# Kernel tuning notes

Measured on AMD Instinct MI355X. Metric: run time of the kernel, lower is better.

## Reference

```python
import jax, jax.numpy as jnp
import numpy as np

VOCAB = 50257
D = 1024
L = 2
EPS = 1e-6


def _attn_layer(x, Wq, bq, Wk, bk, Wv, bv, Wo, bo):
    # x: [b, n, d]; W*: [d, d] (torch Linear convention y = x @ W.T + b)
    Q = jax.nn.elu(x @ Wq.T + bq) + 1.0
    K = jax.nn.elu(x @ Wk.T + bk) + 1.0
    V = x @ Wv.T + bv
    KV = jnp.einsum('bnd,bne->bde', K, V)              # [b, d, d]
    Z = jnp.einsum('bnd,bd->bn', Q, K.sum(axis=1) + EPS)  # [b, n]
    context = jnp.einsum('bnd,bde->bne', Q, KV) / Z[..., None]
    return context @ Wo.T + bo


def setup_inputs() -> dict:
    key = jax.random.key(0)
    ks = jax.random.split(key, 12)
    s = 1.0 / np.sqrt(D)
    inp = {
        'input_ids': jax.random.randint(ks[0], (2, 2048), 0, VOCAB),
        'emb': jax.random.normal(ks[1], (VOCAB, D), jnp.float32) * 0.02,
        'Wq': jax.random.normal(ks[2], (L, D, D), jnp.float32) * s,
        'bq': jnp.zeros((L, D), jnp.float32),
        'Wk': jax.random.normal(ks[3], (L, D, D), jnp.float32) * s,
        'bk': jnp.zeros((L, D), jnp.float32),
        'Wv': jax.random.normal(ks[4], (L, D, D), jnp.float32) * s,
        'bv': jnp.zeros((L, D), jnp.float32),
        'Wo': jax.random.normal(ks[5], (L, D, D), jnp.float32) * s,
        'bo': jnp.zeros((L, D), jnp.float32),
        'W_head': jax.random.normal(ks[6], (VOCAB, D), jnp.float32) * s,
        'b_head': jnp.zeros((VOCAB,), jnp.float32),
    }
    return inp


def reference(input_ids, emb, Wq, bq, Wk, bk, Wv, bv, Wo, bo, W_head, b_head):
    x = emb[input_ids]  # [b, n, d]
    for l in range(L):
        x = _attn_layer(x, Wq[l], bq[l], Wk[l], bk[l], Wv[l], bv[l], Wo[l], bo[l])
    logits = x @ W_head.T + b_head  # [b, n, vocab]
    pooled = x[:, -1]               # [b, d]
    return (logits, pooled)
```

## Files before the change

kernel.cpp:

```cpp
#include <hip/hip_runtime.h>
#include <hip/hip_bf16.h>
#include <math.h>

typedef __bf16 bf8_t __attribute__((ext_vector_type(8)));
typedef __bf16 bf4_t __attribute__((ext_vector_type(4)));
typedef float  f4_t  __attribute__((ext_vector_type(4)));

#define AS_G __attribute__((address_space(1)))
#define AS_L __attribute__((address_space(3)))

static __device__ __forceinline__ void gl_lds16(const __bf16* g, __bf16* l) {
    __builtin_amdgcn_global_load_lds((const AS_G void*)g, (AS_L void*)l, 16, 0, 0);
}

static __device__ __forceinline__ void phase_bar() {
    asm volatile("" ::: "memory");
    __builtin_amdgcn_s_barrier();
    asm volatile("" ::: "memory");
}

enum {
    EPI_NONE = 0,
    EPI_BCOL,
    EPI_BCOL_ELU,
    EPI_BROW,
    EPI_BROW_ELU,
    EPI_ZDIV,
    EPI_BCOL_F32
};

template<int EPI>
__global__ __launch_bounds__(256)
void gemm_bt(const __bf16* __restrict__ A, long lda, long zsA,
             const __bf16* __restrict__ Bt, long ldb, long zsB,
             void* __restrict__ Cv, long ldc, long zsC,
             int M, int N, int K,
             const float* __restrict__ aux, long zsAux)
{
    __shared__ __align__(16) __bf16 tA[128 * 32];
    __shared__ __align__(16) __bf16 tB[128 * 32];

    const int tid  = threadIdx.x;
    const int wave = tid >> 6;
    const int lane = tid & 63;
    const int wm   = (wave >> 1) * 64;
    const int wn   = (wave & 1) * 64;
    const int m0   = blockIdx.y * 128;
    const int n0   = blockIdx.x * 128;
    const long z   = blockIdx.z;

    A  += z * zsA;
    Bt += z * zsB;

    f4_t acc[4][4] = {};

    const int quad = lane >> 4;
    const int l16  = lane & 15;
    const int koff = quad * 8;

    for (int k0 = 0; k0 < K; k0 += 32) {
        #pragma unroll
        for (int p = 0; p < 2; ++p) {
            const int cb = p * 256 + wave * 64;
            const int c  = cb + lane;
            const int r  = c >> 2;
            const int kc = (c & 3) * 8;
            gl_lds16(A + (long)(m0 + r) * lda + (k0 + kc), tA + cb * 8);
            int rb = n0 + r; rb = rb < N ? rb : N - 1;
            gl_lds16(Bt + (long)rb * ldb + (k0 + kc), tB + cb * 8);
        }
        __syncthreads();

        bf8_t af[4], bfr[4];
        #pragma unroll
        for (int i = 0; i < 4; ++i) {
            af[i]  = *(const bf8_t*)(tA + (wm + i * 16 + l16) * 32 + koff);
            bfr[i] = *(const bf8_t*)(tB + (wn + i * 16 + l16) * 32 + koff);
        }
        #pragma unroll
        for (int i = 0; i < 4; ++i)
            #pragma unroll
            for (int j = 0; j < 4; ++j)
                acc[i][j] = __builtin_amdgcn_mfma_f32_16x16x32_bf16(
                    af[i], bfr[j], acc[i][j], 0, 0, 0);
        __syncthreads();
    }

    const float* auxp = aux + z * zsAux;
    float*  Cf = (float*) Cv + z * zsC;
    __bf16* Cb = (__bf16*)Cv + z * zsC;

    #pragma unroll
    for (int i = 0; i < 4; ++i) {
        const int rbase = m0 + wm + i * 16 + quad * 4;
        #pragma unroll
        for (int j = 0; j < 4; ++j) {
            const int col = n0 + wn + j * 16 + l16;
            if (col >= N) continue;
            float bias_c = 0.f;
            if constexpr (EPI == EPI_BCOL || EPI == EPI_BCOL_ELU || EPI == EPI_BCOL_F32)
                bias_c = auxp[col];
            #pragma unroll
            for (int r = 0; r < 4; ++r) {
                const int row = rbase + r;
                if (row >= M) continue;
                float v = acc[i][j][r];
                if constexpr (EPI == EPI_BCOL || EPI == EPI_BCOL_F32) v += bias_c;
                if constexpr (EPI == EPI_BCOL_ELU) {
                    v += bias_c; v = v >= 0.f ? v + 1.f : __expf(v);
                }
                if constexpr (EPI == EPI_BROW) v += auxp[row];
                if constexpr (EPI == EPI_BROW_ELU) {
                    v += auxp[row]; v = v >= 0.f ? v + 1.f : __expf(v);
                }
                if constexpr (EPI == EPI_ZDIV) v /= auxp[row];
                if constexpr (EPI == EPI_BCOL_F32)
                    Cf[(long)row * ldc + col] = v;
                else
                    Cb[(long)row * ldc + col] = (__bf16)v;
            }
        }
    }
}

#define READ_AQ(PTR)                                                          \
    _Pragma("unroll")                                                         \
    for (int ii = 0; ii < 4; ++ii) {                                          \
        const int ro = (wr * 64 + ii * 16 + l16) * 64;                        \
        af[ii][0] = *(const bf8_t*)((PTR) + ro + kx0);                        \
        af[ii][1] = *(const bf8_t*)((PTR) + ro + kx1);                        \
    }

#define READ_BQ(PTR, BQ)                                                      \
    _Pragma("unroll")                                                         \
    for (int jj = 0; jj < 2; ++jj) {                                          \
        const int ro = (wc * 32 + jj * 16 + l16) * 64;                        \
        BQ[jj][0] = *(const bf8_t*)((PTR) + ro + kx0);                        \
        BQ[jj][1] = *(const bf8_t*)((PTR) + ro + kx1);                        \
    }

#define MFMA_QUAD(MB, NB, BQ)                                                 \
    _Pragma("unroll")                                                         \
    for (int ii = 0; ii < 4; ++ii) {                                          \
        _Pragma("unroll")                                                     \
        for (int jj = 0; jj < 2; ++jj) {                                      \
            acc[(MB) + ii][(NB) + jj] = __builtin_amdgcn_mfma_f32_16x16x32_bf16( \
                af[ii][0], BQ[jj][0], acc[(MB) + ii][(NB) + jj], 0, 0, 0);    \
            acc[(MB) + ii][(NB) + jj] = __builtin_amdgcn_mfma_f32_16x16x32_bf16( \
                af[ii][1], BQ[jj][1], acc[(MB) + ii][(NB) + jj], 0, 0, 0);    \
        }                                                                     \
    }

__global__ __launch_bounds__(512)
void gemm256_head(const __bf16* __restrict__ A, int lda,
                  const __bf16* __restrict__ Bt, int ldb,
                  float* __restrict__ C, int ldc,
                  int M, int N, int K, const float* __restrict__ aux)
{
    __shared__ __align__(16) __bf16 sA[2][2][8192];
    __shared__ __align__(16) __bf16 sB[2][2][8192];

    const int tid  = threadIdx.x;
    const int wave = tid >> 6;
    const int lane = tid & 63;
    const int l16  = lane & 15;
    const int quad = lane >> 4;
    const int wr   = wave >> 2;
    const int wc   = wave & 3;

    int id = blockIdx.y * gridDim.x + blockIdx.x;
    const int nwg = gridDim.x * gridDim.y;
    if ((nwg & 7) == 0) {
        const int q = nwg >> 3;
        id = (id & 7) * q + (id >> 3);
    }
    const int m0 = (id % gridDim.x) * 256;
    const int n0 = (id / gridDim.x) * 256;

    const int NT = K >> 6;

    const int l8  = lane >> 3;
    const int gc8 = ((lane & 7) ^ l8) * 8;
    int aoff[2][2], boff[2][2];
    #pragma unroll
    for (int p = 0; p < 2; ++p) {
        const int W  = wave * 2 + p;
        const int rs = W * 8 + l8;
        #pragma unroll
        for (int mq = 0; mq < 2; ++mq) {
            const int m = (rs >> 6) * 128 + mq * 64 + (rs & 63);
            aoff[p][mq] = (m0 + m) * lda + gc8;
        }
        #pragma unroll
        for (int nq = 0; nq < 2; ++nq) {
            int n = n0 + (rs >> 5) * 64 + nq * 32 + (rs & 31);
            n = n < N ? n : N - 1;
            boff[p][nq] = n * ldb + gc8;
        }
    }
    const int W0 = wave * 2, W1 = W0 + 1;

    auto stageA = [&](int kt, int mq) {
        const int ko = (kt < NT ? kt : NT - 1) << 6;
        __bf16* d = &sA[kt & 1][mq][0];
        gl_lds16(A + aoff[0][mq] + ko, d + W0 * 512);
        gl_lds16(A + aoff[1][mq] + ko, d + W1 * 512);
    };
    auto stageB = [&](int kt, int nq) {
        const int ko = (kt < NT ? kt : NT - 1) << 6;
        __bf16* d = &sB[kt & 1][nq][0];
        gl_lds16(Bt + boff[0][nq] + ko, d + W0 * 512);
        gl_lds16(Bt + boff[1][nq] + ko, d + W1 * 512);
    };

    const int kx0 = ((0 + quad) ^ (l16 & 7)) * 8;
    const int kx1 = ((4 + quad) ^ (l16 & 7)) * 8;

    f4_t  acc[8][4] = {};
    bf8_t af[4][2], b0[2][2], b1[2][2];

    stageA(0, 0); stageB(0, 0); stageA(0, 1); stageB(0, 1);
    stageA(1, 0); stageB(1, 0);
    asm volatile("s_waitcnt vmcnt(8)" ::: "memory");
    phase_bar();

    for (int V = 0; V < NT; ++V) {
        const int c = V & 1;
        const __bf16* a0p = &sA[c][0][0];
        const __bf16* a1p = &sA[c][1][0];
        const __bf16* bp0 = &sB[c][0][0];
        const __bf16* bp1 = &sB[c][1][0];

        READ_AQ(a0p)
        READ_BQ(bp0, b0)
        stageA(V + 1, 1);
        phase_bar();
        __builtin_amdgcn_s_setprio(1);
        MFMA_QUAD(0, 0, b0)
        __builtin_amdgcn_s_setprio(0);
        asm volatile("s_waitcnt vmcnt(6)" ::: "memory");
        phase_bar();

        READ_BQ(bp1, b1)
        stageB(V + 1, 1);
        phase_bar();
        __builtin_amdgcn_s_setprio(1);
        MFMA_QUAD(0, 2, b1)
        __builtin_amdgcn_s_setprio(0);
        phase_bar();

        READ_AQ(a1p)
        stageA(V + 2, 0);
        phase_bar();
        __builtin_amdgcn_s_setprio(1);
        MFMA_QUAD(4, 0, b0)
        __builtin_amdgcn_s_setprio(0);
        phase_bar();

        stageB(V + 2, 0);
        phase_bar();
        __builtin_amdgcn_s_setprio(1);
        MFMA_QUAD(4, 2, b1)
        __builtin_amdgcn_s_setprio(0);
        asm volatile("s_waitcnt vmcnt(8)" ::: "memory");
        phase_bar();
    }

    #pragma unroll
    for (int i = 0; i < 8; ++i) {
        const int rbase = m0 + wr * 128 + i * 16 + quad * 4;
        #pragma unroll
        for (int j = 0; j < 4; ++j) {
            const int col = n0 + wc * 64 + j * 16 + l16;
            if (col >= N) continue;
            const float bias = aux[col];
            #pragma unroll
            for (int r = 0; r < 4; ++r)
                C[(long)(rbase + r) * ldc + col] = acc[i][j][r] + bias;
        }
    }
}

__global__ void gather_cast_k(const int* __restrict__ ids,
                              const float* __restrict__ emb,
                              __bf16* __restrict__ x)
{
    const int g = blockIdx.x;
    const long row = (long)ids[g] * 1024;
    f4_t v = ((const f4_t*)(emb + row))[threadIdx.x];
    bf4_t o; o[0]=(__bf16)v[0]; o[1]=(__bf16)v[1]; o[2]=(__bf16)v[2]; o[3]=(__bf16)v[3];
    *(bf4_t*)(x + (long)g * 1024 + threadIdx.x * 4) = o;
}

__global__ void cast_k(const float* __restrict__ w, __bf16* __restrict__ o, long n)
{
    long i = ((long)blockIdx.x * 256 + threadIdx.x) * 4;
    if (i >= n) return;
    f4_t v = *(const f4_t*)(w + i);
    bf4_t b; b[0]=(__bf16)v[0]; b[1]=(__bf16)v[1]; b[2]=(__bf16)v[2]; b[3]=(__bf16)v[3];
    *(bf4_t*)(o + i) = b;
}

__global__ void ksum_k(const __bf16* __restrict__ Kt, float* __restrict__ Ksum)
{
    const int d = blockIdx.x, b = blockIdx.y, t = threadIdx.x;
    const __bf16* rowp = Kt + (long)d * 4096 + b * 2048;
    float s = 0.f;
    for (int i = t; i < 2048; i += 256) s += (float)rowp[i];
    __shared__ float red[256];
    red[t] = s; __syncthreads();
    for (int o = 128; o > 0; o >>= 1) { if (t < o) red[t] += red[t + o]; __syncthreads(); }
    if (t == 0) Ksum[b * 1024 + d] = red[0] + 1e-6f;
}

__global__ void z_k(const __bf16* __restrict__ Q, const float* __restrict__ Ksum,
                    float* __restrict__ Z)
{
    const int n = blockIdx.x, b = blockIdx.y, t = threadIdx.x;
    const __bf16* q = Q + ((long)b * 2048 + n) * 1024;
    const float* ks = Ksum + b * 1024;
    float s = 0.f;
    for (int d = t; d < 1024; d += 256) s += (float)q[d] * ks[d];
    __shared__ float red[256];
    red[t] = s; __syncthreads();
    for (int o = 128; o > 0; o >>= 1) { if (t < o) red[t] += red[t + o]; __syncthreads(); }
    if (t == 0) Z[b * 2048 + n] = red[0];
}

__global__ void pooled_k(const __bf16* __restrict__ x, float* __restrict__ out)
{
    const int b = blockIdx.x, d = threadIdx.x;
    out[b * 1024 + d] = (float)x[((long)b * 2048 + 2047) * 1024 + d];
}

static void launch_gemm(int epi, dim3 grid, hipStream_t s,
                        const __bf16* A, long lda, long zsA,
                        const __bf16* B, long ldb, long zsB,
                        void* C, long ldc, long zsC,
                        int M, int N, int K, const float* aux, long zsAux)
{
    dim3 blk(256);
    switch (epi) {
    case EPI_NONE:     hipLaunchKernelGGL((gemm_bt<EPI_NONE>),     grid, blk, 0, s, A,lda,zsA,B,ldb,zsB,C,ldc,zsC,M,N,K,aux,zsAux); break;
    case EPI_BCOL:     hipLaunchKernelGGL((gemm_bt<EPI_BCOL>),     grid, blk, 0, s, A,lda,zsA,B,ldb,zsB,C,ldc,zsC,M,N,K,aux,zsAux); break;
    case EPI_BCOL_ELU: hipLaunchKernelGGL((gemm_bt<EPI_BCOL_ELU>), grid, blk, 0, s, A,lda,zsA,B,ldb,zsB,C,ldc,zsC,M,N,K,aux,zsAux); break;
    case EPI_BROW:     hipLaunchKernelGGL((gemm_bt<EPI_BROW>),     grid, blk, 0, s, A,lda,zsA,B,ldb,zsB,C,ldc,zsC,M,N,K,aux,zsAux); break;
    case EPI_BROW_ELU: hipLaunchKernelGGL((gemm_bt<EPI_BROW_ELU>), grid, blk, 0, s, A,lda,zsA,B,ldb,zsB,C,ldc,zsC,M,N,K,aux,zsAux); break;
    case EPI_ZDIV:     hipLaunchKernelGGL((gemm_bt<EPI_ZDIV>),     grid, blk, 0, s, A,lda,zsA,B,ldb,zsB,C,ldc,zsC,M,N,K,aux,zsAux); break;
    case EPI_BCOL_F32: hipLaunchKernelGGL((gemm_bt<EPI_BCOL_F32>), grid, blk, 0, s, A,lda,zsA,B,ldb,zsB,C,ldc,zsC,M,N,K,aux,zsAux); break;
    }
}

extern "C" void kernel_launch(void* const* d_in, const int* in_sizes, int n_in,
                              void* d_out, int out_size, void* d_ws, size_t ws_size,
                              hipStream_t stream)
{
    const int*   ids = (const int*)  d_in[0];
    const float* emb = (const float*)d_in[1];
    const float* Wq  = (const float*)d_in[2];
    const float* bq  = (const float*)d_in[3];
    const float* Wk  = (const float*)d_in[4];
    const float* bk  = (const float*)d_in[5];
    const float* Wv  = (const float*)d_in[6];
    const float* bv  = (const float*)d_in[7];
    const float* Wo  = (const float*)d_in[8];
    const float* bo  = (const float*)d_in[9];
    const float* Wh  = (const float*)d_in[10];
    const float* bh  = (const float*)d_in[11];
    float* out = (float*)d_out;

    __bf16* x_bf   = (__bf16*)d_ws;
    __bf16* Q_bf   = x_bf   + 4194304;
    __bf16* Kt_bf  = Q_bf   + 4194304;
    __bf16* Vt_bf  = Kt_bf  + 4194304;
    __bf16* KVt_bf = Vt_bf  + 4194304;
    __bf16* ctx_bf = KVt_bf + 2097152;
    __bf16* Wq_bf  = ctx_bf + 4194304;
    __bf16* Wk_bf  = Wq_bf  + 2097152;
    __bf16* Wv_bf  = Wk_bf  + 2097152;
    __bf16* Wo_bf  = Wv_bf  + 2097152;
    __bf16* Wh_bf  = Wo_bf  + 2097152;
    float*  Ksum   = (float*)(Wh_bf + 51463168);
    float*  Z      = Ksum + 2048;

    auto castn = [&](const float* src, __bf16* dst, long n) {
        int blocks = (int)((n / 4 + 255) / 256);
        hipLaunchKernelGGL(cast_k, dim3(blocks), dim3(256), 0, stream, src, dst, n);
    };
    castn(Wq, Wq_bf, 2097152);
    castn(Wk, Wk_bf, 2097152);
    castn(Wv, Wv_bf, 2097152);
    castn(Wo, Wo_bf, 2097152);
    castn(Wh, Wh_bf, 51463168);
    hipLaunchKernelGGL(gather_cast_k, dim3(4096), dim3(256), 0, stream, ids, emb, x_bf);

    for (int l = 0; l < 2; ++l) {
        const __bf16 *wq = Wq_bf + l * 1048576, *wk = Wk_bf + l * 1048576,
                     *wv = Wv_bf + l * 1048576, *wo = Wo_bf + l * 1048576;
        const float *bql = bq + l * 1024, *bkl = bk + l * 1024,
                    *bvl = bv + l * 1024, *bol = bo + l * 1024;

        launch_gemm(EPI_BCOL_ELU, dim3(8, 32, 1), stream,
                    x_bf, 1024, 0, wq, 1024, 0, Q_bf, 1024, 0,
                    4096, 1024, 1024, bql, 0);
        launch_gemm(EPI_BROW_ELU, dim3(32, 8, 1), stream,
                    wk, 1024, 0, x_bf, 1024, 0, Kt_bf, 4096, 0,
                    1024, 4096, 1024, bkl, 0);
        launch_gemm(EPI_BROW, dim3(32, 8, 1), stream,
                    wv, 1024, 0, x_bf, 1024, 0, Vt_bf, 4096, 0,
                    1024, 4096, 1024, bvl, 0);
        hipLaunchKernelGGL(ksum_k, dim3(1024, 2), dim3(256), 0, stream, Kt_bf, Ksum);
        launch_gemm(EPI_NONE, dim3(8, 8, 2), stream,
                    Vt_bf, 4096, 2048, Kt_bf, 4096, 2048, KVt_bf, 1024, 1048576,
                    1024, 1024, 2048, Ksum, 0);
        hipLaunchKernelGGL(z_k, dim3(2048, 2), dim3(256), 0, stream, Q_bf, Ksum, Z);
        launch_gemm(EPI_ZDIV, dim3(8, 16, 2), stream,
                    Q_bf, 1024, 2097152, KVt_bf, 1024, 1048576, ctx_bf, 1024, 2097152,
                    2048, 1024, 1024, Z, 2048);
        launch_gemm(EPI_BCOL, dim3(8, 32, 1), stream,
                    ctx_bf, 1024, 0, wo, 1024, 0, x_bf, 1024, 0,
                    4096, 1024, 1024, bol, 0);
    }

    hipLaunchKernelGGL(gemm256_head, dim3(16, 197), dim3(512), 0, stream,
                       x_bf, 1024, Wh_bf, 1024, out, 50257,
                       4096, 50257, 1024, bh);
    hipLaunchKernelGGL(pooled_k, dim3(2), dim3(1024), 0, stream,
                       x_bf, out + (long)4096 * 50257);
}
```

Baseline: 2.120 ms.

## Multi-stage LDS pipeline in generic GEMM and nontemporal stores for head logits

Converts the generic bf16 GEMM main loop from single-buffered load/sync/compute into a 5-slot LDS ring with three tiles prefetched ahead, waiting on vmcnt instead of two __syncthreads per k-step. The aim is to overlap global-to-LDS loads with MFMA work. The head GEMM epilogue now writes its fp32 logits with nontemporal stores to reduce cache pollution from the large output. LDS use grows to 80KB per block, which may reduce occupancy, and the out-of-range prefetch clamp re-reads the last tile.

```diff
diff --git a/kernel.cpp b/kernel.cpp
--- a/kernel.cpp
+++ b/kernel.cpp
@@ -37,8 +37,8 @@
              int M, int N, int K,
              const float* __restrict__ aux, long zsAux)
 {
-    __shared__ __align__(16) __bf16 tA[128 * 32];
-    __shared__ __align__(16) __bf16 tB[128 * 32];
+    __shared__ __align__(16) __bf16 tA[5][128 * 32];
+    __shared__ __align__(16) __bf16 tB[5][128 * 32];
 
     const int tid  = threadIdx.x;
     const int wave = tid >> 6;
@@ -52,30 +52,44 @@
     A  += z * zsA;
     Bt += z * zsB;
 
-    f4_t acc[4][4] = {};
-
     const int quad = lane >> 4;
     const int l16  = lane & 15;
     const int koff = quad * 8;
-
-    for (int k0 = 0; k0 < K; k0 += 32) {
+    const int NT   = K >> 5;
+
+    auto stage = [&](int st) {
+        const int kk = st < NT ? st : NT - 1;
+        const int k0 = kk << 5;
+        __bf16* dA = &tA[st % 5][0];
+        __bf16* dB = &tB[st % 5][0];
         #pragma unroll
         for (int p = 0; p < 2; ++p) {
             const int cb = p * 256 + wave * 64;
             const int c  = cb + lane;
             const int r  = c >> 2;
             const int kc = (c & 3) * 8;
-            gl_lds16(A + (long)(m0 + r) * lda + (k0 + kc), tA + cb * 8);
+            gl_lds16(A + (long)(m0 + r) * lda + (k0 + kc), dA + cb * 8);
             int rb = n0 + r; rb = rb < N ? rb : N - 1;
-            gl_lds16(Bt + (long)rb * ldb + (k0 + kc), tB + cb * 8);
-        }
-        __syncthreads();
-
+            gl_lds16(Bt + (long)rb * ldb + (k0 + kc), dB + cb * 8);
+        }
+    };
+
+    f4_t acc[4][4] = {};
+
+    stage(0); stage(1); stage(2);
+
+    for (int kt = 0; kt < NT; ++kt) {
+        stage(kt + 3);
+        asm volatile("s_waitcnt vmcnt(12)" ::: "memory");
+        phase_bar();
+
+        const __bf16* pA = &tA[kt % 5][0];
+        const __bf16* pB = &tB[kt % 5][0];
         bf8_t af[4], bfr[4];
         #pragma unroll
         for (int i = 0; i < 4; ++i) {
-            af[i]  = *(const bf8_t*)(tA + (wm + i * 16 + l16) * 32 + koff);
-            bfr[i] = *(const bf8_t*)(tB + (wn + i * 16 + l16) * 32 + koff);
+            af[i]  = *(const bf8_t*)(pA + (wm + i * 16 + l16) * 32 + koff);
+            bfr[i] = *(const bf8_t*)(pB + (wn + i * 16 + l16) * 32 + koff);
         }
         #pragma unroll
         for (int i = 0; i < 4; ++i)
@@ -83,7 +97,6 @@
             for (int j = 0; j < 4; ++j)
                 acc[i][j] = __builtin_amdgcn_mfma_f32_16x16x32_bf16(
                     af[i], bfr[j], acc[i][j], 0, 0, 0);
-        __syncthreads();
     }
 
     const float* auxp = aux + z * zsAux;
@@ -276,7 +289,8 @@
             const float bias = aux[col];
             #pragma unroll
             for (int r = 0; r < 4; ++r)
-                C[(long)(rbase + r) * ldc + col] = acc[i][j][r] + bias;
+                __builtin_nontemporal_store(acc[i][j][r] + bias,
+                                            &C[(long)(rbase + r) * ldc + col]);
         }
     }
 }
```

Result: slower. 2.443 ms (+15.3%).
